# Optimization experiments

Measured on AMD Instinct MI355X. Metric: run time of the kernel, lower is better.

## Reference

```python
import jax, jax.numpy as jnp
import numpy as np

N_KERNELS = 11
B, Q, D, E, C = 128, 32, 512, 300, 128

def _kernel_mus(n):
    mus = [1.0]
    bs = 2.0 / (n - 1)
    mus.append(1 - bs / 2)
    for i in range(1, n - 1):
        mus.append(mus[i] - bs)
    return np.array(mus, dtype=np.float32)

def _kernel_sigmas(n):
    bs = 2.0 / (n - 1)
    return np.array([0.001] + [0.5 * bs] * (n - 1), dtype=np.float32)

def setup_inputs():
    key = jax.random.key(0)
    ks = jax.random.split(key, 10)
    return {
        "query_embeddings": jax.random.normal(ks[0], (B, Q, E), jnp.float32),
        "document_embeddings": jax.random.normal(ks[1], (B, D, E), jnp.float32),
        "query_pad_oov_mask": jnp.ones((B, Q), jnp.float32),
        "document_pad_oov_mask": jnp.ones((B, D), jnp.float32),
        "conv1_w": jax.random.normal(ks[2], (C, E, 1), jnp.float32) * 0.05,
        "conv1_b": jnp.zeros((C,), jnp.float32),
        "conv2_w": jax.random.normal(ks[3], (C, E, 2), jnp.float32) * 0.05,
        "conv2_b": jnp.zeros((C,), jnp.float32),
        "conv3_w": jax.random.normal(ks[4], (C, E, 3), jnp.float32) * 0.05,
        "conv3_b": jnp.zeros((C,), jnp.float32),
        "nn_scaler": jnp.full((1,), 0.01, jnp.float32),
        "dense_w": jax.random.uniform(ks[5], (1, N_KERNELS * 9), jnp.float32, -0.014, 0.014),
        "dense_b": jnp.zeros((1,), jnp.float32),
        "dense_mean_w": jax.random.normal(ks[6], (1, N_KERNELS * 9), jnp.float32) * 0.05,
        "dense_mean_b": jnp.zeros((1,), jnp.float32),
        "dense_comb_w": jax.random.normal(ks[7], (1, 2), jnp.float32) * 0.5,
    }

def _conv_relu(x, w, b):
    # x: [B, L, E] -> [B, L, C]; right-pad by k-1 (ConstantPad1d((0, k-1))) so out len == L
    k = w.shape[-1]
    y = jax.lax.conv_general_dilated(x.transpose(0, 2, 1), w, (1,), [(0, k - 1)],
                                     dimension_numbers=("NCH", "OIH", "NCH"))
    return jax.nn.relu(y + b[None, :, None]).transpose(0, 2, 1)

def _kernel_pool(q, d, qd_mask, q_mask, doc_len, mu, sigma, scaler):
    # cosine matrix (AllenNLP CosineMatrixAttention: L2-normalize with 1e-13 tie-break)
    qn = q / (jnp.linalg.norm(q, axis=-1, keepdims=True) + 1e-13)
    dn = d / (jnp.linalg.norm(d, axis=-1, keepdims=True) + 1e-13)
    cos = jnp.einsum("bqc,bdc->bqd", qn, dn) * qd_mask
    # RBF soft-histogram kernels over the similarity matrix: [B,q,d,K]
    kr = jnp.exp(-(cos[..., None] - mu) ** 2 / (2.0 * sigma ** 2)) * qd_mask[..., None]
    pkq = kr.sum(axis=2)  # [B, Q, K]
    std = (jnp.log(jnp.clip(pkq, 1e-10)) * scaler * q_mask[..., None]).sum(axis=1)
    pkq_mean = pkq / doc_len[:, None, None]
    mean = (jnp.log(jnp.clip(pkq_mean, 1e-10)) * scaler * q_mask[..., None]).sum(axis=1)
    return std, mean

def _forward(qe, de, qm, dm, c1w, c1b, c2w, c2b, c3w, c3b, ns, dw, db, dmw, dmb, dcw):
    mu = jnp.asarray(_kernel_mus(N_KERNELS))
    sigma = jnp.asarray(_kernel_sigmas(N_KERNELS))
    qd_mask = qm[:, :, None] * dm[:, None, :]
    doc_len = dm.sum(axis=1)
    convs = [(c1w, c1b), (c2w, c2b), (c3w, c3b)]
    q_res = [_conv_relu(qe, w, b) for w, b in convs]
    d_res = [_conv_relu(de, w, b) for w, b in convs]
    std_list, mean_list = [], []
    for qr in q_res:
        for dr in d_res:
            s, m = _kernel_pool(qr, dr, qd_mask, qm, doc_len, mu, sigma, ns)
            std_list.append(s)
            mean_list.append(m)
    all_grams = jnp.concatenate(std_list, axis=1)       # [B, 9*K]
    all_grams_mean = jnp.concatenate(mean_list, axis=1)
    dense_out = all_grams @ dw.T + db
    dense_mean_out = all_grams_mean @ dmw.T + dmb
    comb = jnp.concatenate([dense_out, dense_mean_out], axis=1) @ dcw.T
    return comb[:, 0]

def reference(query_embeddings, document_embeddings, query_pad_oov_mask, document_pad_oov_mask,
              conv1_w, conv1_b, conv2_w, conv2_b, conv3_w, conv3_b,
              nn_scaler, dense_w, dense_b, dense_mean_w, dense_mean_b, dense_comb_w):
    return _forward(query_embeddings, document_embeddings, query_pad_oov_mask, document_pad_oov_mask,
                    conv1_w, conv1_b, conv2_w, conv2_b, conv3_w, conv3_b,
                    nn_scaler, dense_w, dense_b, dense_mean_w, dense_mean_b, dense_comb_w)
```

## Files before the change

### kernel.cpp

```cpp
#include <hip/hip_runtime.h>
#include <hip/hip_bf16.h>
#include <cstdint>

namespace {

typedef __bf16 bf8v __attribute__((ext_vector_type(8)));
typedef __bf16 bf4v __attribute__((ext_vector_type(4)));
typedef float  f4v  __attribute__((ext_vector_type(4)));

constexpr int kB = 128;
constexpr int kQ = 32;
constexpr int kD = 512;
constexpr int kE = 300;
constexpr int kC = 128;
constexpr int kK = 11;

constexpr size_t QNB_B = 491520;
constexpr size_t DNB_B = 3637248;
constexpr size_t PKQ_B = 53968896;

constexpr float LOG2E = 1.4426950408889634f;

constexpr int XS_STRIDE = 344;

__global__ __launch_bounds__(256) void prep_kernel(
    const float* __restrict__ w1, const float* __restrict__ w2, const float* __restrict__ w3,
    __bf16* __restrict__ wb)
{
  int i = blockIdx.x * 256 + threadIdx.x;
  if (i >= 245760) return;
  int el = i & 31;
  int sc = i >> 5;
  int c  = sc & 127;
  int sk = sc >> 7;
  int slab = sk / 10;
  int ks = sk - slab * 10;
  int e = ks * 32 + el;
  float v = 0.f;
  if (e < kE) {
    if (slab == 0)      v = w1[c * kE + e];
    else if (slab <= 2) v = w2[(c * kE + e) * 2 + (slab - 1)];
    else                v = w3[(c * kE + e) * 3 + (slab - 3)];
  }
  wb[i] = (__bf16)v;
}

template<int KF>
__device__ __forceinline__ void conv_slab(
    const __bf16* __restrict__ wslab,
    const __bf16* __restrict__ Xs,
    int lr, int g, int wm, int wn, f4v acc[2][4])
{
  const int arow = wm * 32 + lr;
  const __bf16* wl = wslab + (size_t)(wn * 64 + lr) * 32 + g * 8;

  bf8v An[2], Wn[4];
  #pragma unroll
  for (int mf = 0; mf < 2; ++mf)
    An[mf] = *(const bf8v*)&Xs[(arow + mf * 16) * XS_STRIDE + g * 8];
  #pragma unroll
  for (int nf = 0; nf < 4; ++nf)
    Wn[nf] = *(const bf8v*)(wl + (size_t)(nf * 16) * 32);

  for (int ks = 0; ks < 10; ++ks) {
    #pragma unroll
    for (int j = 0; j < KF; ++j) {
      bf8v Ac[2] = { An[0], An[1] };
      bf8v Wc[4] = { Wn[0], Wn[1], Wn[2], Wn[3] };
      const int jn  = (j + 1 == KF) ? 0 : j + 1;
      const int ksn = (j + 1 == KF) ? ks + 1 : ks;
      if (ksn < 10) {
        #pragma unroll
        for (int mf = 0; mf < 2; ++mf)
          An[mf] = *(const bf8v*)&Xs[(arow + mf * 16 + jn) * XS_STRIDE + ksn * 32 + g * 8];
        #pragma unroll
        for (int nf = 0; nf < 4; ++nf)
          Wn[nf] = *(const bf8v*)(wl + ((size_t)(jn * 10 + ksn) * 128 + nf * 16) * 32);
      }
      #pragma unroll
      for (int nf = 0; nf < 4; ++nf) {
        acc[0][nf] = __builtin_amdgcn_mfma_f32_16x16x32_bf16(Ac[0], Wc[nf], acc[0][nf], 0, 0, 0);
        acc[1][nf] = __builtin_amdgcn_mfma_f32_16x16x32_bf16(Ac[1], Wc[nf], acc[1][nf], 0, 0, 0);
      }
    }
  }
}

__global__ __launch_bounds__(256, 3) void conv_fused(
    const float* __restrict__ qe, const float* __restrict__ de,
    const __bf16* __restrict__ wb,
    const float* __restrict__ b1, const float* __restrict__ b2, const float* __restrict__ b3,
    __bf16* __restrict__ qnb, __bf16* __restrict__ dnb)
{
  const int bx = blockIdx.x;
  const int b  = blockIdx.y;
  const bool isq = (bx == 0);
  const int L  = isq ? kQ : kD;
  const int p0 = isq ? 0 : (bx - 1) * 64;
  const float* xsrc = (isq ? qe : de) + (size_t)b * L * kE;

  const int t = threadIdx.x;
  const int w = t >> 6, l = t & 63;
  const int wm = w & 1, wn = w >> 1;
  const int lr = l & 15, g = l >> 4;

  __shared__ __align__(16) __bf16 Xs[66 * XS_STRIDE];
  __shared__ float sqs[2][64];

  for (int idx = t; idx < 66 * 82; idx += 256) {
    int row = idx / 82, c4 = idx - row * 82;
    int gp = p0 + row;
    float4 v = make_float4(0.f, 0.f, 0.f, 0.f);
    if (gp < L && c4 < 75) v = *(const float4*)(xsrc + (size_t)gp * kE + c4 * 4);
    bf4v hv = { (__bf16)v.x, (__bf16)v.y, (__bf16)v.z, (__bf16)v.w };
    *(bf4v*)&Xs[row * XS_STRIDE + c4 * 4] = hv;
  }
  __syncthreads();

  #pragma unroll
  for (int c0 = 0; c0 < 3; ++c0) {
    f4v acc[2][4];
    #pragma unroll
    for (int mf = 0; mf < 2; ++mf)
      #pragma unroll
      for (int nf = 0; nf < 4; ++nf)
        acc[mf][nf] = (f4v)0.f;

    if (c0 == 0)      conv_slab<1>(wb,           Xs, lr, g, wm, wn, acc);
    else if (c0 == 1) conv_slab<2>(wb + 40960,   Xs, lr, g, wm, wn, acc);
    else              conv_slab<3>(wb + 122880,  Xs, lr, g, wm, wn, acc);

    const float* bias = (c0 == 0) ? b1 : ((c0 == 1) ? b2 : b3);
    float bvs[4];
    #pragma unroll
    for (int nf = 0; nf < 4; ++nf) bvs[nf] = bias[wn * 64 + nf * 16 + lr];

    f4v ssum[2];
    #pragma unroll
    for (int mf = 0; mf < 2; ++mf) {
      ssum[mf] = (f4v)0.f;
      #pragma unroll
      for (int nf = 0; nf < 4; ++nf)
        #pragma unroll
        for (int r = 0; r < 4; ++r) {
          float y = fmaxf(acc[mf][nf][r] + bvs[nf], 0.f);
          acc[mf][nf][r] = y;
          ssum[mf][r] += y * y;
        }
    }
    #pragma unroll
    for (int off = 1; off < 16; off <<= 1)
      #pragma unroll
      for (int mf = 0; mf < 2; ++mf)
        #pragma unroll
        for (int r = 0; r < 4; ++r)
          ssum[mf][r] += __shfl_xor(ssum[mf][r], off);

    __syncthreads();
    if (lr == 0) {
      #pragma unroll
      for (int mf = 0; mf < 2; ++mf)
        *(float4*)&sqs[wn][wm * 32 + mf * 16 + g * 4] = *(float4*)&ssum[mf];
    }
    __syncthreads();
    f4v inv[2];
    #pragma unroll
    for (int mf = 0; mf < 2; ++mf) {
      float4 o = *(const float4*)&sqs[1 - wn][wm * 32 + mf * 16 + g * 4];
      inv[mf][0] = 1.f / (sqrtf(ssum[mf][0] + o.x) + 1e-13f);
      inv[mf][1] = 1.f / (sqrtf(ssum[mf][1] + o.y) + 1e-13f);
      inv[mf][2] = 1.f / (sqrtf(ssum[mf][2] + o.z) + 1e-13f);
      inv[mf][3] = 1.f / (sqrtf(ssum[mf][3] + o.w) + 1e-13f);
    }
    __bf16* outp = (isq ? qnb : dnb) + ((size_t)(c0 * kB + b)) * L * kC;
    #pragma unroll
    for (int mf = 0; mf < 2; ++mf) {
      #pragma unroll
      for (int r = 0; r < 4; ++r) {
        int gp = p0 + wm * 32 + mf * 16 + g * 4 + r;
        if (gp < L) {
          #pragma unroll
          for (int nf = 0; nf < 4; ++nf) {
            int c = wn * 64 + nf * 16 + lr;
            outp[(size_t)gp * kC + c] = (__bf16)(acc[mf][nf][r] * inv[mf][r]);
          }
        }
      }
    }
  }
}

__global__ __launch_bounds__(256) void pool_mfma(
    const __bf16* __restrict__ qnb,
    const __bf16* __restrict__ dnb,
    const float* __restrict__ qmask,
    const float* __restrict__ dmask,
    float* __restrict__ pkq)
{
  const int pair = blockIdx.x;
  const int b = blockIdx.y;
  const int qi = pair / 3, dj = pair - qi * 3;
  const __bf16* qb = qnb + ((size_t)qi * kB + b) * kQ * kC;
  const __bf16* db = dnb + ((size_t)dj * kB + b) * kD * kC;

  const int t = threadIdx.x;
  const int w = t >> 6, l = t & 63;
  const int lr = l & 15, g = l >> 4;

  __shared__ float red[4][2][16][kK];

  bf8v Bq[2][4];
  #pragma unroll
  for (int qt = 0; qt < 2; ++qt)
    #pragma unroll
    for (int kc = 0; kc < 4; ++kc)
      Bq[qt][kc] = *(const bf8v*)&qb[(size_t)(qt * 16 + lr) * kC + kc * 32 + g * 8];

  float qmv[2];
  #pragma unroll
  for (int qt = 0; qt < 2; ++qt) qmv[qt] = qmask[b * kQ + qt * 16 + lr];

  const float c1[10] = { 129.84255368f, 100.98865286f,  72.13475204f,  43.28085123f,  14.42695041f,
                         -14.42695041f, -43.28085123f, -72.13475204f, -100.98865286f, -129.84255368f };
  const float c2[10] = { -58.42914915f, -35.34602850f, -18.03368801f, -6.49212768f, -0.72134752f,
                          -0.72134752f,  -6.49212768f, -18.03368801f, -35.34602850f, -58.42914915f };
  const float C50 = -50.f * LOG2E;
  const float C0  = -500000.f * LOG2E;

  float pk[2][kK];
  #pragma unroll
  for (int qt = 0; qt < 2; ++qt)
    #pragma unroll
    for (int k = 0; k < kK; ++k) pk[qt][k] = 0.f;

  const int dt0 = w * 8;
  bf8v An[4];
  #pragma unroll
  for (int kc = 0; kc < 4; ++kc)
    An[kc] = *(const bf8v*)&db[(size_t)(dt0 * 16 + lr) * kC + kc * 32 + g * 8];

  for (int dtl = 0; dtl < 8; ++dtl) {
    const int drow0 = (dt0 + dtl) * 16;
    bf8v Ac[4];
    #pragma unroll
    for (int kc = 0; kc < 4; ++kc) Ac[kc] = An[kc];
    if (dtl < 7) {
      #pragma unroll
      for (int kc = 0; kc < 4; ++kc)
        An[kc] = *(const bf8v*)&db[(size_t)(drow0 + 16 + lr) * kC + kc * 32 + g * 8];
    }
    f4v acc0 = (f4v)0.f, acc1 = (f4v)0.f;
    #pragma unroll
    for (int kc = 0; kc < 4; ++kc) {
      acc0 = __builtin_amdgcn_mfma_f32_16x16x32_bf16(Ac[kc], Bq[0][kc], acc0, 0, 0, 0);
      acc1 = __builtin_amdgcn_mfma_f32_16x16x32_bf16(Ac[kc], Bq[1][kc], acc1, 0, 0, 0);
    }
    float4 dmv = *(const float4*)&dmask[b * kD + drow0 + g * 4];
    #pragma unroll
    for (int qt = 0; qt < 2; ++qt) {
      const f4v& a = qt ? acc1 : acc0;
      #pragma unroll
      for (int r = 0; r < 4; ++r) {
        float dm = (r == 0) ? dmv.x : (r == 1) ? dmv.y : (r == 2) ? dmv.z : dmv.w;
        float off = fmaf(dm, 1000.f, -1000.f);
        float s = a[r] * qmv[qt] * dm;
        float s2 = s * s;
        float base = fmaf(s2, C50, off);
        float dd = s - 1.f;
        pk[qt][0] += exp2f(fmaf(dd * dd, C0, off));
        #pragma unroll
        for (int k = 0; k < 10; ++k)
          pk[qt][k + 1] += exp2f(fmaf(c1[k], s, base) + c2[k]);
      }
    }
  }

  #pragma unroll
  for (int off = 16; off < 64; off <<= 1)
    #pragma unroll
    for (int qt = 0; qt < 2; ++qt)
      #pragma unroll
      for (int k = 0; k < kK; ++k)
        pk[qt][k] += __shfl_xor(pk[qt][k], off);

  if (l < 16) {
    #pragma unroll
    for (int qt = 0; qt < 2; ++qt)
      #pragma unroll
      for (int k = 0; k < kK; ++k)
        red[w][qt][lr][k] = pk[qt][k];
  }
  __syncthreads();
  for (int i = t; i < 2 * 16 * kK; i += 256) {
    int qt = i / (16 * kK);
    int rem = i - qt * 16 * kK;
    int lq = rem / kK, k = rem - lq * kK;
    float v = red[0][qt][lq][k] + red[1][qt][lq][k] + red[2][qt][lq][k] + red[3][qt][lq][k];
    int q = qt * 16 + lq;
    pkq[(((size_t)pair * kB + b) * kQ + q) * kK + k] = v * qmask[b * kQ + q];
  }
}

__global__ __launch_bounds__(128) void finalize_kernel(
    const float* __restrict__ pkq, const float* __restrict__ qmask,
    const float* __restrict__ dmask, const float* __restrict__ nsp,
    const float* __restrict__ dw, const float* __restrict__ dbp,
    const float* __restrict__ dmw, const float* __restrict__ dmbp,
    const float* __restrict__ dcw, float* __restrict__ out)
{
  const int b = blockIdx.x;
  const int t = threadIdx.x;
  __shared__ float sh[4];
  float dl = 0.f;
  for (int d = t; d < kD; d += 128) dl += dmask[b * kD + d];
  #pragma unroll
  for (int off = 1; off < 64; off <<= 1) dl += __shfl_xor(dl, off);
  if ((t & 63) == 0) sh[t >> 6] = dl;
  __syncthreads();
  const float idl = 1.f / (sh[0] + sh[1]);
  const float sc = nsp[0];
  float ps = 0.f, pm = 0.f;
  for (int i = t; i < 99; i += 128) {
    int pr = i / kK, kk = i - pr * kK;
    const float* base = pkq + ((size_t)pr * kB + b) * kQ * kK + kk;
    float ss = 0.f, sm = 0.f;
    for (int q = 0; q < kQ; ++q) {
      float v = base[q * kK];
      float qq = qmask[b * kQ + q];
      ss += __logf(fmaxf(v, 1e-10f)) * qq;
      sm += __logf(fmaxf(v * idl, 1e-10f)) * qq;
    }
    ps += dw[i] * ss;
    pm += dmw[i] * sm;
  }
  ps *= sc; pm *= sc;
  #pragma unroll
  for (int off = 1; off < 64; off <<= 1) { ps += __shfl_xor(ps, off); pm += __shfl_xor(pm, off); }
  __syncthreads();
  if ((t & 63) == 0) { sh[t >> 6] = ps; sh[2 + (t >> 6)] = pm; }
  __syncthreads();
  if (t == 0) {
    float PS = sh[0] + sh[1] + dbp[0];
    float PM = sh[2] + sh[3] + dmbp[0];
    out[b] = dcw[0] * PS + dcw[1] * PM;
  }
}

}

extern "C" void kernel_launch(void* const* d_in, const int* in_sizes, int n_in,
                              void* d_out, int out_size, void* d_ws, size_t ws_size,
                              hipStream_t stream) {
  const float* qe  = (const float*)d_in[0];
  const float* de  = (const float*)d_in[1];
  const float* qm  = (const float*)d_in[2];
  const float* dm  = (const float*)d_in[3];
  const float* w1  = (const float*)d_in[4];
  const float* b1  = (const float*)d_in[5];
  const float* w2  = (const float*)d_in[6];
  const float* b2  = (const float*)d_in[7];
  const float* w3  = (const float*)d_in[8];
  const float* b3  = (const float*)d_in[9];
  const float* ns  = (const float*)d_in[10];
  const float* dw  = (const float*)d_in[11];
  const float* db  = (const float*)d_in[12];
  const float* dmw = (const float*)d_in[13];
  const float* dmb = (const float*)d_in[14];
  const float* dcw = (const float*)d_in[15];
  float* out = (float*)d_out;

  char* wsb = (char*)d_ws;
  __bf16* wb  = (__bf16*)wsb;
  __bf16* qnb = (__bf16*)(wsb + QNB_B);
  __bf16* dnb = (__bf16*)(wsb + DNB_B);
  float*  pkq = (float*)(wsb + PKQ_B);

  prep_kernel<<<960, 256, 0, stream>>>(w1, w2, w3, wb);
  conv_fused<<<dim3(9, kB), 256, 0, stream>>>(qe, de, wb, b1, b2, b3, qnb, dnb);
  pool_mfma<<<dim3(9, kB), 256, 0, stream>>>(qnb, dnb, qm, dm, pkq);
  finalize_kernel<<<kB, 128, 0, stream>>>(pkq, qm, dm, ns, dw, db, dmw, dmb, dcw, out);
}
```

Measured before the change: 183.2 us.

## Stage conv weight tiles through double-buffered LDS with register prefetch

The conv kernel used to have every wave read its bf16 weight fragments directly from global memory, so the two M-waves fetched the same weight tile twice. Now the 256 threads cooperatively load each 128x32 weight k-slice into registers two steps ahead and write it into a padded, double-buffered LDS tile. All waves then read their MFMA B-operands from LDS, which cuts redundant global/L2 traffic. The cost is a __syncthreads after every k-step (8 MFMAs per barrier), extra LDS use that may lower blocks per CU, and removal of the min-blocks launch bound hint.

```diff
diff --git a/kernel.cpp b/kernel.cpp
--- a/kernel.cpp
+++ b/kernel.cpp
@@ -22,6 +22,7 @@
 constexpr float LOG2E = 1.4426950408889634f;
 
 constexpr int XS_STRIDE = 344;
+constexpr int WS_STRIDE = 40;
 
 __global__ __launch_bounds__(256) void prep_kernel(
     const float* __restrict__ w1, const float* __restrict__ w2, const float* __restrict__ w3,
@@ -45,48 +46,38 @@
   wb[i] = (__bf16)v;
 }
 
-template<int KF>
-__device__ __forceinline__ void conv_slab(
-    const __bf16* __restrict__ wslab,
+__device__ __forceinline__ void conv_step(
     const __bf16* __restrict__ Xs,
-    int lr, int g, int wm, int wn, f4v acc[2][4])
+    const __bf16* __restrict__ Wcur, __bf16* __restrict__ Wnxt,
+    const uint4* __restrict__ wsrc, bool issue_next, bool do_write,
+    uint4& ra, uint4& rb, uint4& na, uint4& nb,
+    int u0, int u1, int wst0, int wst1,
+    int a0, int a1, int wfoff, f4v (&acc)[2][4])
 {
-  const int arow = wm * 32 + lr;
-  const __bf16* wl = wslab + (size_t)(wn * 64 + lr) * 32 + g * 8;
-
-  bf8v An[2], Wn[4];
-  #pragma unroll
-  for (int mf = 0; mf < 2; ++mf)
-    An[mf] = *(const bf8v*)&Xs[(arow + mf * 16) * XS_STRIDE + g * 8];
-  #pragma unroll
-  for (int nf = 0; nf < 4; ++nf)
-    Wn[nf] = *(const bf8v*)(wl + (size_t)(nf * 16) * 32);
-
-  for (int ks = 0; ks < 10; ++ks) {
-    #pragma unroll
-    for (int j = 0; j < KF; ++j) {
-      bf8v Ac[2] = { An[0], An[1] };
-      bf8v Wc[4] = { Wn[0], Wn[1], Wn[2], Wn[3] };
-      const int jn  = (j + 1 == KF) ? 0 : j + 1;
-      const int ksn = (j + 1 == KF) ? ks + 1 : ks;
-      if (ksn < 10) {
-        #pragma unroll
-        for (int mf = 0; mf < 2; ++mf)
-          An[mf] = *(const bf8v*)&Xs[(arow + mf * 16 + jn) * XS_STRIDE + ksn * 32 + g * 8];
-        #pragma unroll
-        for (int nf = 0; nf < 4; ++nf)
-          Wn[nf] = *(const bf8v*)(wl + ((size_t)(jn * 10 + ksn) * 128 + nf * 16) * 32);
-      }
-      #pragma unroll
-      for (int nf = 0; nf < 4; ++nf) {
-        acc[0][nf] = __builtin_amdgcn_mfma_f32_16x16x32_bf16(Ac[0], Wc[nf], acc[0][nf], 0, 0, 0);
-        acc[1][nf] = __builtin_amdgcn_mfma_f32_16x16x32_bf16(Ac[1], Wc[nf], acc[1][nf], 0, 0, 0);
-      }
-    }
-  }
-}
-
-__global__ __launch_bounds__(256, 3) void conv_fused(
+  if (issue_next) { na = wsrc[u0]; nb = wsrc[u1]; }
+  bf8v A0 = *(const bf8v*)(Xs + a0);
+  bf8v A1 = *(const bf8v*)(Xs + a1);
+  const __bf16* wp = Wcur + wfoff;
+  bf8v W0 = *(const bf8v*)(wp);
+  bf8v W1 = *(const bf8v*)(wp + 16 * WS_STRIDE);
+  bf8v W2 = *(const bf8v*)(wp + 32 * WS_STRIDE);
+  bf8v W3 = *(const bf8v*)(wp + 48 * WS_STRIDE);
+  acc[0][0] = __builtin_amdgcn_mfma_f32_16x16x32_bf16(A0, W0, acc[0][0], 0, 0, 0);
+  acc[1][0] = __builtin_amdgcn_mfma_f32_16x16x32_bf16(A1, W0, acc[1][0], 0, 0, 0);
+  acc[0][1] = __builtin_amdgcn_mfma_f32_16x16x32_bf16(A0, W1, acc[0][1], 0, 0, 0);
+  acc[1][1] = __builtin_amdgcn_mfma_f32_16x16x32_bf16(A1, W1, acc[1][1], 0, 0, 0);
+  acc[0][2] = __builtin_amdgcn_mfma_f32_16x16x32_bf16(A0, W2, acc[0][2], 0, 0, 0);
+  acc[1][2] = __builtin_amdgcn_mfma_f32_16x16x32_bf16(A1, W2, acc[1][2], 0, 0, 0);
+  acc[0][3] = __builtin_amdgcn_mfma_f32_16x16x32_bf16(A0, W3, acc[0][3], 0, 0, 0);
+  acc[1][3] = __builtin_amdgcn_mfma_f32_16x16x32_bf16(A1, W3, acc[1][3], 0, 0, 0);
+  if (do_write) {
+    *(uint4*)(Wnxt + wst0) = ra;
+    *(uint4*)(Wnxt + wst1) = rb;
+  }
+  __syncthreads();
+}
+
+__global__ __launch_bounds__(256) void conv_fused(
     const float* __restrict__ qe, const float* __restrict__ de,
     const __bf16* __restrict__ wb,
     const float* __restrict__ b1, const float* __restrict__ b2, const float* __restrict__ b3,
@@ -105,7 +96,18 @@
   const int lr = l & 15, g = l >> 4;
 
   __shared__ __align__(16) __bf16 Xs[66 * XS_STRIDE];
+  __shared__ __align__(16) __bf16 Wbuf[2][128 * WS_STRIDE];
   __shared__ float sqs[2][64];
+
+  const int u0 = t, u1 = t + 256;
+  const int wst0 = (t >> 2) * WS_STRIDE + (t & 3) * 8;
+  const int wst1 = ((t >> 2) + 64) * WS_STRIDE + (t & 3) * 8;
+  const int wfoff = (wn * 64 + lr) * WS_STRIDE + g * 8;
+  const uint4* wsrcb = (const uint4*)wb;
+
+  uint4 r0a, r0b, r1a, r1b;
+  r0a = wsrcb[u0];        r0b = wsrcb[u1];
+  r1a = wsrcb[512 + u0];  r1b = wsrcb[512 + u1];
 
   for (int idx = t; idx < 66 * 82; idx += 256) {
     int row = idx / 82, c4 = idx - row * 82;
@@ -115,10 +117,12 @@
     bf4v hv = { (__bf16)v.x, (__bf16)v.y, (__bf16)v.z, (__bf16)v.w };
     *(bf4v*)&Xs[row * XS_STRIDE + c4 * 4] = hv;
   }
-  __syncthreads();
-
-  #pragma unroll
-  for (int c0 = 0; c0 < 3; ++c0) {
+  *(uint4*)(&Wbuf[0][0] + wst0) = r0a;
+  *(uint4*)(&Wbuf[0][0] + wst1) = r0b;
+  __syncthreads();
+
+  #pragma unroll
+  for (int grp = 0; grp < 3; ++grp) {
     f4v acc[2][4];
     #pragma unroll
     for (int mf = 0; mf < 2; ++mf)
@@ -126,11 +130,27 @@
       for (int nf = 0; nf < 4; ++nf)
         acc[mf][nf] = (f4v)0.f;
 
-    if (c0 == 0)      conv_slab<1>(wb,           Xs, lr, g, wm, wn, acc);
-    else if (c0 == 1) conv_slab<2>(wb + 40960,   Xs, lr, g, wm, wn, acc);
-    else              conv_slab<3>(wb + 122880,  Xs, lr, g, wm, wn, acc);
-
-    const float* bias = (c0 == 0) ? b1 : ((c0 == 1) ? b2 : b3);
+    #pragma unroll
+    for (int j = 0; j <= grp; ++j) {
+      const int slab = grp * (grp + 1) / 2 + j;
+      const int abase = (wm * 32 + lr + j) * XS_STRIDE + g * 8;
+      #pragma unroll
+      for (int ks = 0; ks < 10; ++ks) {
+        const int s = slab * 10 + ks;
+        const bool issue = (s + 2 < 60);
+        const bool wr    = (s + 1 < 60);
+        const int a0 = abase + ks * 32;
+        const int a1 = a0 + 16 * XS_STRIDE;
+        if ((s & 1) == 0)
+          conv_step(Xs, &Wbuf[0][0], &Wbuf[1][0], wsrcb + (size_t)(s + 2) * 512, issue, wr,
+                    r1a, r1b, r0a, r0b, u0, u1, wst0, wst1, a0, a1, wfoff, acc);
+        else
+          conv_step(Xs, &Wbuf[1][0], &Wbuf[0][0], wsrcb + (size_t)(s + 2) * 512, issue, wr,
+                    r0a, r0b, r1a, r1b, u0, u1, wst0, wst1, a0, a1, wfoff, acc);
+      }
+    }
+
+    const float* bias = (grp == 0) ? b1 : ((grp == 1) ? b2 : b3);
     float bvs[4];
     #pragma unroll
     for (int nf = 0; nf < 4; ++nf) bvs[nf] = bias[wn * 64 + nf * 16 + lr];
@@ -172,7 +192,7 @@
       inv[mf][2] = 1.f / (sqrtf(ssum[mf][2] + o.z) + 1e-13f);
       inv[mf][3] = 1.f / (sqrtf(ssum[mf][3] + o.w) + 1e-13f);
     }
-    __bf16* outp = (isq ? qnb : dnb) + ((size_t)(c0 * kB + b)) * L * kC;
+    __bf16* outp = (isq ? qnb : dnb) + ((size_t)(grp * kB + b)) * L * kC;
     #pragma unroll
     for (int mf = 0; mf < 2; ++mf) {
       #pragma unroll
```

After: 162.4 us. 11.3% less time.
